# Optimization experiments

Measured on AMD Instinct MI355X. Metric: run time of the kernel, lower is better.

Reference implementation:

```python
import jax, jax.numpy as jnp
import numpy as np

B, C, L = 32, 256, 4096
CM = C // 8  # intermediate channels
EPS = 1e-5


def _conv1x1(v, w, b):
    # v: [B, Cin, L], w: [Cout, Cin], b: [Cout]
    return jnp.einsum('bcl,oc->bol', v, w) + b[None, :, None]


def _bn(v, gamma, beta, mean, var):
    # eval-mode BatchNorm1d over channel dim; v: [B, Ch, L]
    inv = gamma / jnp.sqrt(var + EPS)
    return v * inv[None, :, None] + (beta - mean * inv)[None, :, None]


def setup_inputs() -> dict:
    key = jax.random.key(0)
    ks = jax.random.split(key, 28)
    s = lambda fan: 1.0 / np.sqrt(fan)

    def bn_params(k, ch):
        k1, k2, k3, k4 = jax.random.split(k, 4)
        return (jax.random.normal(k1, (ch,)) * 0.1 + 1.0,   # gamma
                jax.random.normal(k2, (ch,)) * 0.1,          # beta
                jax.random.normal(k3, (ch,)) * 0.1,          # running mean
                jax.random.uniform(k4, (ch,)) + 0.5)         # running var (>0)

    lg1, lbe1, lm1, lv1 = bn_params(ks[2], CM)
    lg2, lbe2, lm2, lv2 = bn_params(ks[5], C)
    gg1, gbe1, gm1, gv1 = bn_params(ks[8], CM)
    gg2, gbe2, gm2, gv2 = bn_params(ks[11], C)

    return dict(
        x=jax.random.normal(ks[0], (B, C, L), dtype=jnp.float32),
        y=jax.random.normal(ks[1], (B, C, L), dtype=jnp.float32),
        lw1=jax.random.uniform(ks[12], (CM, C), minval=-s(C), maxval=s(C)),
        lb1=jax.random.uniform(ks[13], (CM,), minval=-s(C), maxval=s(C)),
        lg1=lg1, lbe1=lbe1, lm1=lm1, lv1=lv1,
        lw2=jax.random.uniform(ks[14], (C, CM), minval=-s(CM), maxval=s(CM)),
        lb2=jax.random.uniform(ks[15], (C,), minval=-s(CM), maxval=s(CM)),
        lg2=lg2, lbe2=lbe2, lm2=lm2, lv2=lv2,
        gw1=jax.random.uniform(ks[16], (CM, C), minval=-s(C), maxval=s(C)),
        gb1=jax.random.uniform(ks[17], (CM,), minval=-s(C), maxval=s(C)),
        gg1=gg1, gbe1=gbe1, gm1=gm1, gv1=gv1,
        gw2=jax.random.uniform(ks[18], (C, CM), minval=-s(CM), maxval=s(CM)),
        gb2=jax.random.uniform(ks[19], (C,), minval=-s(CM), maxval=s(CM)),
        gg2=gg2, gbe2=gbe2, gm2=gm2, gv2=gv2,
    )


def reference(x, y,
              lw1, lb1, lg1, lbe1, lm1, lv1,
              lw2, lb2, lg2, lbe2, lm2, lv2,
              gw1, gb1, gg1, gbe1, gm1, gv1,
              gw2, gb2, gg2, gbe2, gm2, gv2):
    combined = x + y  # [B, C, L]

    # local branch: conv1x1 -> BN -> ReLU -> conv1x1 -> BN
    la = _bn(_conv1x1(combined, lw1, lb1), lg1, lbe1, lm1, lv1)
    la = jax.nn.relu(la)
    la = _bn(_conv1x1(la, lw2, lb2), lg2, lbe2, lm2, lv2)  # [B, C, L]

    # global branch: AdaptiveMaxPool1d(1) -> conv1x1 -> BN -> ReLU -> conv1x1 -> BN
    ga = jnp.max(combined, axis=2, keepdims=True)  # [B, C, 1]
    ga = _bn(_conv1x1(ga, gw1, gb1), gg1, gbe1, gm1, gv1)
    ga = jax.nn.relu(ga)
    ga = _bn(_conv1x1(ga, gw2, gb2), gg2, gbe2, gm2, gv2)  # [B, C, 1]

    att = jax.nn.sigmoid(la + ga)  # broadcast over L
    return 2.0 * x * att + 2.0 * y * (1.0 - att)
```

## Files before the change

### kernel.cpp

```cpp
#include <hip/hip_runtime.h>
#include <hip/hip_bf16.h>


#define NB 32
#define NC 256
#define NM 32
#define NL 4096
#define BNEPS 1e-5f

#define LT1 128
#define KST 128
#define LDW 132
#define LT2 64

typedef unsigned int u32;
typedef unsigned short u16;
typedef __attribute__((ext_vector_type(8))) short bf16x8;
typedef __attribute__((ext_vector_type(4))) float f32x4;

#define OFF_AF1  0
#define OFF_AF2  (OFF_AF1 + 4096)
#define OFF_B1F  (OFF_AF2 + 4096)
#define OFF_B2F  (OFF_B1F + NM)
#define OFF_GW1T (OFF_B2F + NC)
#define OFF_GB1F (OFF_GW1T + NC*NM)
#define OFF_GW2T (OFF_GB1F + NM)
#define OFF_GB2F (OFF_GW2T + NM*NC)
#define OFF_AC   (OFF_GB2F + NC)
#define OFF_GMAX (OFF_AC + NB*NC)
#define OFF_HC   (OFF_GMAX + NB*NC)

__device__ __forceinline__ unsigned f2u_mono(float f) {
    unsigned u = __float_as_uint(f);
    return (u & 0x80000000u) ? ~u : (u | 0x80000000u);
}
__device__ __forceinline__ float u2f_mono(unsigned u) {
    return (u & 0x80000000u) ? __uint_as_float(u & 0x7fffffffu)
                             : __uint_as_float(~u);
}
__device__ __forceinline__ u16 f2bf(float a) {
    return __bfloat16_as_ushort(__float2bfloat16(a));
}
__device__ __forceinline__ float bf2f(u16 a) {
    return __uint_as_float(((u32)a) << 16);
}
__device__ __forceinline__ u32 pack2(float a, float b) {
    return (u32)f2bf(a) | ((u32)f2bf(b) << 16);
}

__global__ __launch_bounds__(256) void k_fold(
    const float* __restrict__ lw1, const float* __restrict__ lb1,
    const float* __restrict__ lg1, const float* __restrict__ lbe1,
    const float* __restrict__ lm1, const float* __restrict__ lv1,
    const float* __restrict__ lw2, const float* __restrict__ lb2,
    const float* __restrict__ lg2, const float* __restrict__ lbe2,
    const float* __restrict__ lm2, const float* __restrict__ lv2,
    const float* __restrict__ gw1, const float* __restrict__ gb1,
    const float* __restrict__ gg1, const float* __restrict__ gbe1,
    const float* __restrict__ gm1, const float* __restrict__ gv1,
    const float* __restrict__ gw2, const float* __restrict__ gb2,
    const float* __restrict__ gg2, const float* __restrict__ gbe2,
    const float* __restrict__ gm2, const float* __restrict__ gv2,
    float* __restrict__ ws) {
    u16* af1   = (u16*)(ws + OFF_AF1);
    u16* af2   = (u16*)(ws + OFF_AF2);
    float* b1f  = ws + OFF_B1F;  float* b2f  = ws + OFF_B2F;
    float* gw1t = ws + OFF_GW1T; float* gb1f = ws + OFF_GB1F;
    float* gw2t = ws + OFF_GW2T; float* gb2f = ws + OFF_GB2F;
    unsigned* gmaxU = (unsigned*)(ws + OFF_GMAX);

    int tid = blockIdx.x * blockDim.x + threadIdx.x;
    int nt  = gridDim.x * blockDim.x;

    for (int i = tid; i < 8192; i += nt) {
        int j = i & 7, lane = (i >> 3) & 63, q = (i >> 9) & 7, mt = i >> 12;
        int m = 16 * mt + (lane & 15);
        int c = 32 * q + 8 * (lane >> 4) + j;
        float inv = lg1[m] * rsqrtf(lv1[m] + BNEPS);
        af1[i] = f2bf(lw1[m * NC + c] * inv);
    }
    for (int i = tid; i < 8192; i += nt) {
        int j = i & 7, lane = (i >> 3) & 63, ct = i >> 9;
        int cout = 16 * ct + (lane & 15);
        int m = 8 * (lane >> 4) + j;
        float inv = lg2[cout] * rsqrtf(lv2[cout] + BNEPS);
        af2[i] = f2bf(lw2[cout * NM + m] * inv);
    }
    for (int i = tid; i < NC * NM; i += nt) {
        int c = i >> 5, m = i & 31;
        float gi1 = gg1[m] * rsqrtf(gv1[m] + BNEPS);
        gw1t[c * NM + m] = gw1[m * NC + c] * gi1;
        float gi2 = gg2[c] * rsqrtf(gv2[c] + BNEPS);
        gw2t[m * NC + c] = gw2[c * NM + m] * gi2;
    }
    for (int i = tid; i < NM; i += nt) {
        float inv = lg1[i] * rsqrtf(lv1[i] + BNEPS);
        b1f[i] = lb1[i] * inv + lbe1[i] - lm1[i] * inv;
        float gi = gg1[i] * rsqrtf(gv1[i] + BNEPS);
        gb1f[i] = gb1[i] * gi + gbe1[i] - gm1[i] * gi;
    }
    for (int i = tid; i < NC; i += nt) {
        float inv = lg2[i] * rsqrtf(lv2[i] + BNEPS);
        b2f[i] = lb2[i] * inv + lbe2[i] - lm2[i] * inv;
        float gi = gg2[i] * rsqrtf(gv2[i] + BNEPS);
        gb2f[i] = gb2[i] * gi + gbe2[i] - gm2[i] * gi;
    }
    for (int i = tid; i < NB * NC; i += nt) gmaxU[i] = 0u;
}

__global__ __launch_bounds__(256, 4) void k_pass1(
    const float4* __restrict__ x4, const float4* __restrict__ y4,
    const u16* __restrict__ af1, const float* __restrict__ b1f,
    unsigned* __restrict__ gmaxU, u16* __restrict__ hc) {
    __shared__ u16 vt[KST * LDW];
    __shared__ float cmax[256];
    int b   = blockIdx.y;
    int l0  = blockIdx.x * LT1;
    int tid = threadIdx.x;
    int w = tid >> 6, lane = tid & 63, g = lane >> 4, li = lane & 15;

    bf16x8 a1[2][8];
#pragma unroll
    for (int mt = 0; mt < 2; ++mt)
#pragma unroll
        for (int q = 0; q < 8; ++q)
            a1[mt][q] = *(const bf16x8*)(af1 + (((mt * 8 + q) * 64) + lane) * 8);

    f32x4 acc[2][2];
#pragma unroll
    for (int mt = 0; mt < 2; ++mt)
#pragma unroll
        for (int t = 0; t < 2; ++t) {
            f32x4 z = {0.f, 0.f, 0.f, 0.f};
            acc[mt][t] = z;
        }

    int hw = tid >> 5;
    int lq = tid & 31;

#pragma unroll
    for (int s = 0; s < 2; ++s) {
#pragma unroll 4
        for (int it = 0; it < 16; ++it) {
            int cc = it * 8 + hw;
            int c  = s * KST + cc;
            size_t ridx = ((size_t)(b * NC + c)) * (NL / 4) + (l0 / 4) + lq;
            float4 xv = x4[ridx];
            float4 yv = y4[ridx];
            float v0 = xv.x + yv.x, v1 = xv.y + yv.y;
            float v2 = xv.z + yv.z, v3 = xv.w + yv.w;
            uint2 wv;
            wv.x = pack2(v0, v1);
            wv.y = pack2(v2, v3);
            *(uint2*)&vt[cc * LDW + 4 * lq] = wv;
        }
        __syncthreads();

#pragma unroll
        for (int qq = 0; qq < 4; ++qq)
#pragma unroll
            for (int t = 0; t < 2; ++t) {
                int lcol = 32 * w + 16 * t + li;
                bf16x8 bf;
#pragma unroll
                for (int j = 0; j < 8; ++j)
                    bf[j] = (short)vt[(32 * qq + 8 * g + j) * LDW + lcol];
                acc[0][t] = __builtin_amdgcn_mfma_f32_16x16x32_bf16(
                    a1[0][s * 4 + qq], bf, acc[0][t], 0, 0, 0);
                acc[1][t] = __builtin_amdgcn_mfma_f32_16x16x32_bf16(
                    a1[1][s * 4 + qq], bf, acc[1][t], 0, 0, 0);
            }

        {
            int cc = tid & 127, half = tid >> 7;
            float mx = -3.402823466e38f;
            int base = cc * LDW + half * 64;
#pragma unroll 8
            for (int l = 0; l < 64; ++l)
                mx = fmaxf(mx, bf2f(vt[base + l]));
            cmax[tid] = mx;
        }
        __syncthreads();
        if (tid < 128)
            atomicMax(&gmaxU[b * NC + s * KST + tid],
                      f2u_mono(fmaxf(cmax[tid], cmax[tid + 128])));
    }

#pragma unroll
    for (int mt = 0; mt < 2; ++mt)
#pragma unroll
        for (int t = 0; t < 2; ++t) {
            int l  = l0 + 32 * w + 16 * t + li;
            int m0 = 16 * mt + 4 * g;
            float h0 = fmaxf(acc[mt][t][0] + b1f[m0 + 0], 0.f);
            float h1 = fmaxf(acc[mt][t][1] + b1f[m0 + 1], 0.f);
            float h2 = fmaxf(acc[mt][t][2] + b1f[m0 + 2], 0.f);
            float h3 = fmaxf(acc[mt][t][3] + b1f[m0 + 3], 0.f);
            uint2 st;
            st.x = pack2(h0, h1);
            st.y = pack2(h2, h3);
            *(uint2*)&hc[((size_t)b * NL + l) * NM + m0] = st;
        }
}

__global__ __launch_bounds__(256) void k_global(
    const float* __restrict__ gw1t, const float* __restrict__ gb1f,
    const float* __restrict__ gw2t, const float* __restrict__ gb2f,
    const float* __restrict__ b2f, const unsigned* __restrict__ gmaxU,
    float* __restrict__ ac) {
    __shared__ float smax[NC];
    __shared__ float g1[NM];
    int b = blockIdx.x;
    int t = threadIdx.x;
    smax[t] = u2f_mono(gmaxU[b * NC + t]);
    __syncthreads();
    if (t < NM) {
        float a = gb1f[t];
        for (int c = 0; c < NC; ++c) a = fmaf(gw1t[c * NM + t], smax[c], a);
        g1[t] = fmaxf(a, 0.f);
    }
    __syncthreads();
    float a = b2f[t] + gb2f[t];
#pragma unroll
    for (int m = 0; m < NM; ++m) a = fmaf(gw2t[m * NC + t], g1[m], a);
    ac[b * NC + t] = a;
}

__global__ __launch_bounds__(256, 4) void k_pass2(
    const float* __restrict__ x, const float* __restrict__ y,
    const u16* __restrict__ af2, const float* __restrict__ ac,
    const u16* __restrict__ hc, float* __restrict__ out) {
    __shared__ float acl[NC];
    int b   = blockIdx.y;
    int l0  = blockIdx.x * LT2;
    int tid = threadIdx.x;
    int w = tid >> 6, lane = tid & 63, g = lane >> 4, li = lane & 15;

    acl[tid] = ac[b * NC + tid];

    bf16x8 a2[4];
#pragma unroll
    for (int ct = 0; ct < 4; ++ct)
        a2[ct] = *(const bf16x8*)(af2 + ((w * 4 + ct) * 64 + lane) * 8);
    __syncthreads();

#pragma unroll 2
    for (int lt = 0; lt < 4; ++lt) {
        int l = l0 + 16 * lt + li;
        bf16x8 bfrag = *(const bf16x8*)(hc + ((size_t)b * NL + l) * NM + 8 * g);
        f32x4 acc[4];
#pragma unroll
        for (int ct = 0; ct < 4; ++ct) {
            f32x4 z = {0.f, 0.f, 0.f, 0.f};
            acc[ct] = __builtin_amdgcn_mfma_f32_16x16x32_bf16(
                a2[ct], bfrag, z, 0, 0, 0);
        }
#pragma unroll
        for (int ct = 0; ct < 4; ++ct)
#pragma unroll
            for (int r = 0; r < 4; ++r) {
                int cout = 64 * w + 16 * ct + 4 * g + r;
                float z = acc[ct][r] + acl[cout];
                float att = 1.f / (1.f + __expf(-z));
                size_t idx = ((size_t)(b * NC + cout)) * NL + l;
                float xv = x[idx];
                float yv = y[idx];
                float tt = yv + att * (xv - yv);
                out[idx] = tt + tt;
            }
    }
}

extern "C" void kernel_launch(void* const* d_in, const int* in_sizes, int n_in,
                              void* d_out, int out_size, void* d_ws,
                              size_t ws_size, hipStream_t stream) {
    (void)in_sizes; (void)n_in; (void)out_size; (void)ws_size;
    const float* x = (const float*)d_in[0];
    const float* y = (const float*)d_in[1];
    float* ws  = (float*)d_ws;
    float* out = (float*)d_out;

    u16* af1   = (u16*)(ws + OFF_AF1);
    u16* af2   = (u16*)(ws + OFF_AF2);
    float* b1f  = ws + OFF_B1F;  float* b2f  = ws + OFF_B2F;
    float* gw1t = ws + OFF_GW1T; float* gb1f = ws + OFF_GB1F;
    float* gw2t = ws + OFF_GW2T; float* gb2f = ws + OFF_GB2F;
    float* ac   = ws + OFF_AC;
    unsigned* gmaxU = (unsigned*)(ws + OFF_GMAX);
    u16* hc = (u16*)(ws + OFF_HC);

    k_fold<<<64, 256, 0, stream>>>(
        (const float*)d_in[2],  (const float*)d_in[3],  (const float*)d_in[4],
        (const float*)d_in[5],  (const float*)d_in[6],  (const float*)d_in[7],
        (const float*)d_in[8],  (const float*)d_in[9],  (const float*)d_in[10],
        (const float*)d_in[11], (const float*)d_in[12], (const float*)d_in[13],
        (const float*)d_in[14], (const float*)d_in[15], (const float*)d_in[16],
        (const float*)d_in[17], (const float*)d_in[18], (const float*)d_in[19],
        (const float*)d_in[20], (const float*)d_in[21], (const float*)d_in[22],
        (const float*)d_in[23], (const float*)d_in[24], (const float*)d_in[25],
        ws);
    k_pass1<<<dim3(NL / LT1, NB), 256, 0, stream>>>(
        (const float4*)x, (const float4*)y, af1, b1f, gmaxU, hc);
    k_global<<<NB, 256, 0, stream>>>(gw1t, gb1f, gw2t, gb2f, b2f, gmaxU, ac);
    k_pass2<<<dim3(NL / LT2, NB), 256, 0, stream>>>(
        x, y, af2, ac, hc, out);
}
```

Measured before the change: 479.2 us.

## Fuse second conv into first pass and stream blend over bf16 pre-activations

The second 1x1 conv now runs inside the first kernel from a shared-memory hidden tile, and the full 256-channel pre-activation is stored as bf16 in channel-major layout. A separate elementwise blend kernel then reads x, y and the pre-activation with vectorized, coalesced float4 loads and applies sigmoid and the mix. The aim is to replace the strided scalar loads of the old second pass with streaming access. In exchange it adds a large intermediate buffer (extra global write and read traffic), and the work is split into batch halves when the workspace is too small.

```diff
diff --git a/kernel.cpp b/kernel.cpp
--- a/kernel.cpp
+++ b/kernel.cpp
@@ -7,11 +7,9 @@
 #define NM 32
 #define NL 4096
 #define BNEPS 1e-5f
-
 #define LT1 128
-#define KST 128
 #define LDW 132
-#define LT2 64
+#define HLW 40
 
 typedef unsigned int u32;
 typedef unsigned short u16;
@@ -28,7 +26,7 @@
 #define OFF_GB2F (OFF_GW2T + NM*NC)
 #define OFF_AC   (OFF_GB2F + NC)
 #define OFF_GMAX (OFF_AC + NB*NC)
-#define OFF_HC   (OFF_GMAX + NB*NC)
+#define OFF_Z    (OFF_GMAX + NB*NC)
 
 __device__ __forceinline__ unsigned f2u_mono(float f) {
     unsigned u = __float_as_uint(f);
@@ -108,56 +106,55 @@
     for (int i = tid; i < NB * NC; i += nt) gmaxU[i] = 0u;
 }
 
-__global__ __launch_bounds__(256, 4) void k_pass1(
+__global__ __launch_bounds__(256, 4) void k_conv(
     const float4* __restrict__ x4, const float4* __restrict__ y4,
-    const u16* __restrict__ af1, const float* __restrict__ b1f,
-    unsigned* __restrict__ gmaxU, u16* __restrict__ hc) {
-    __shared__ u16 vt[KST * LDW];
+    const u16* __restrict__ af1, const u16* __restrict__ af2,
+    const float* __restrict__ b1f, unsigned* __restrict__ gmaxU,
+    u32* __restrict__ z2, int b_off) {
+    __shared__ u16 vt[64 * LDW];
+    __shared__ u16 hl[128 * HLW];
     __shared__ float cmax[256];
-    int b   = blockIdx.y;
-    int l0  = blockIdx.x * LT1;
-    int tid = threadIdx.x;
+    int brel = blockIdx.y;
+    int b    = b_off + brel;
+    int l0   = blockIdx.x * LT1;
+    int tid  = threadIdx.x;
     int w = tid >> 6, lane = tid & 63, g = lane >> 4, li = lane & 15;
-
-    bf16x8 a1[2][8];
+    int hw = tid >> 5, lq = tid & 31;
+
+    f32x4 acc[2][2];
 #pragma unroll
     for (int mt = 0; mt < 2; ++mt)
 #pragma unroll
-        for (int q = 0; q < 8; ++q)
-            a1[mt][q] = *(const bf16x8*)(af1 + (((mt * 8 + q) * 64) + lane) * 8);
-
-    f32x4 acc[2][2];
-#pragma unroll
-    for (int mt = 0; mt < 2; ++mt)
-#pragma unroll
         for (int t = 0; t < 2; ++t) {
-            f32x4 z = {0.f, 0.f, 0.f, 0.f};
-            acc[mt][t] = z;
-        }
-
-    int hw = tid >> 5;
-    int lq = tid & 31;
-
-#pragma unroll
-    for (int s = 0; s < 2; ++s) {
-#pragma unroll 4
-        for (int it = 0; it < 16; ++it) {
+            f32x4 zr = {0.f, 0.f, 0.f, 0.f};
+            acc[mt][t] = zr;
+        }
+
+    for (int s = 0; s < 4; ++s) {
+        bf16x8 a1[2][2];
+#pragma unroll
+        for (int mt = 0; mt < 2; ++mt)
+#pragma unroll
+            for (int qq = 0; qq < 2; ++qq)
+                a1[mt][qq] = *(const bf16x8*)(
+                    af1 + (((mt * 8 + 2 * s + qq) * 64) + lane) * 8);
+
+#pragma unroll
+        for (int it = 0; it < 8; ++it) {
             int cc = it * 8 + hw;
-            int c  = s * KST + cc;
-            size_t ridx = ((size_t)(b * NC + c)) * (NL / 4) + (l0 / 4) + lq;
+            int c  = s * 64 + cc;
+            size_t ridx = ((size_t)(b * NC + c)) * (NL / 4) + (l0 >> 2) + lq;
             float4 xv = x4[ridx];
             float4 yv = y4[ridx];
-            float v0 = xv.x + yv.x, v1 = xv.y + yv.y;
-            float v2 = xv.z + yv.z, v3 = xv.w + yv.w;
             uint2 wv;
-            wv.x = pack2(v0, v1);
-            wv.y = pack2(v2, v3);
+            wv.x = pack2(xv.x + yv.x, xv.y + yv.y);
+            wv.y = pack2(xv.z + yv.z, xv.w + yv.w);
             *(uint2*)&vt[cc * LDW + 4 * lq] = wv;
         }
         __syncthreads();
 
 #pragma unroll
-        for (int qq = 0; qq < 4; ++qq)
+        for (int qq = 0; qq < 2; ++qq)
 #pragma unroll
             for (int t = 0; t < 2; ++t) {
                 int lcol = 32 * w + 16 * t + li;
@@ -166,31 +163,33 @@
                 for (int j = 0; j < 8; ++j)
                     bf[j] = (short)vt[(32 * qq + 8 * g + j) * LDW + lcol];
                 acc[0][t] = __builtin_amdgcn_mfma_f32_16x16x32_bf16(
-                    a1[0][s * 4 + qq], bf, acc[0][t], 0, 0, 0);
+                    a1[0][qq], bf, acc[0][t], 0, 0, 0);
                 acc[1][t] = __builtin_amdgcn_mfma_f32_16x16x32_bf16(
-                    a1[1][s * 4 + qq], bf, acc[1][t], 0, 0, 0);
+                    a1[1][qq], bf, acc[1][t], 0, 0, 0);
             }
 
         {
-            int cc = tid & 127, half = tid >> 7;
+            int cc = tid & 63, q4 = tid >> 6;
+            int base = cc * LDW + 32 * q4;
             float mx = -3.402823466e38f;
-            int base = cc * LDW + half * 64;
 #pragma unroll 8
-            for (int l = 0; l < 64; ++l)
+            for (int l = 0; l < 32; ++l)
                 mx = fmaxf(mx, bf2f(vt[base + l]));
             cmax[tid] = mx;
         }
         __syncthreads();
-        if (tid < 128)
-            atomicMax(&gmaxU[b * NC + s * KST + tid],
-                      f2u_mono(fmaxf(cmax[tid], cmax[tid + 128])));
+        if (tid < 64) {
+            float m0 = fmaxf(fmaxf(cmax[tid], cmax[tid + 64]),
+                             fmaxf(cmax[tid + 128], cmax[tid + 192]));
+            atomicMax(&gmaxU[b * NC + s * 64 + tid], f2u_mono(m0));
+        }
     }
 
 #pragma unroll
     for (int mt = 0; mt < 2; ++mt)
 #pragma unroll
         for (int t = 0; t < 2; ++t) {
-            int l  = l0 + 32 * w + 16 * t + li;
+            int l  = 32 * w + 16 * t + li;
             int m0 = 16 * mt + 4 * g;
             float h0 = fmaxf(acc[mt][t][0] + b1f[m0 + 0], 0.f);
             float h1 = fmaxf(acc[mt][t][1] + b1f[m0 + 1], 0.f);
@@ -199,18 +198,46 @@
             uint2 st;
             st.x = pack2(h0, h1);
             st.y = pack2(h2, h3);
-            *(uint2*)&hc[((size_t)b * NL + l) * NM + m0] = st;
-        }
+            *(uint2*)&hl[l * HLW + m0] = st;
+        }
+    __syncthreads();
+
+    for (int r = 0; r < 4; ++r) {
+#pragma unroll
+        for (int c4 = 0; c4 < 4; ++c4) {
+            int ct = 4 * r + c4;
+            bf16x8 a2 = *(const bf16x8*)(af2 + (ct * 64 + lane) * 8);
+#pragma unroll
+            for (int t = 0; t < 2; ++t) {
+                int l = 32 * w + 16 * t + li;
+                bf16x8 hb = *(const bf16x8*)&hl[l * HLW + 8 * g];
+                f32x4 zz = {0.f, 0.f, 0.f, 0.f};
+                zz = __builtin_amdgcn_mfma_f32_16x16x32_bf16(a2, hb, zz, 0, 0, 0);
+#pragma unroll
+                for (int rr = 0; rr < 4; ++rr)
+                    vt[(16 * c4 + 4 * g + rr) * LDW + l] = f2bf(zz[rr]);
+            }
+        }
+        __syncthreads();
+#pragma unroll
+        for (int i = 0; i < 16; ++i) {
+            int row  = 16 * w + i;
+            int cout = 64 * r + row;
+            u32 v = *(const u32*)&vt[row * LDW + 2 * lane];
+            z2[(((size_t)brel * NC + cout) * NL + l0) / 2 + lane] = v;
+        }
+        __syncthreads();
+    }
 }
 
 __global__ __launch_bounds__(256) void k_global(
     const float* __restrict__ gw1t, const float* __restrict__ gb1f,
     const float* __restrict__ gw2t, const float* __restrict__ gb2f,
     const float* __restrict__ b2f, const unsigned* __restrict__ gmaxU,
-    float* __restrict__ ac) {
+    float* __restrict__ ac, int b_off) {
     __shared__ float smax[NC];
     __shared__ float g1[NM];
-    int b = blockIdx.x;
+    int b = b_off + blockIdx.x;
     int t = threadIdx.x;
     smax[t] = u2f_mono(gmaxU[b * NC + t]);
     __syncthreads();
@@ -226,55 +253,44 @@
     ac[b * NC + t] = a;
 }
 
-__global__ __launch_bounds__(256, 4) void k_pass2(
-    const float* __restrict__ x, const float* __restrict__ y,
-    const u16* __restrict__ af2, const float* __restrict__ ac,
-    const u16* __restrict__ hc, float* __restrict__ out) {
-    __shared__ float acl[NC];
-    int b   = blockIdx.y;
-    int l0  = blockIdx.x * LT2;
-    int tid = threadIdx.x;
-    int w = tid >> 6, lane = tid & 63, g = lane >> 4, li = lane & 15;
-
-    acl[tid] = ac[b * NC + tid];
-
-    bf16x8 a2[4];
-#pragma unroll
-    for (int ct = 0; ct < 4; ++ct)
-        a2[ct] = *(const bf16x8*)(af2 + ((w * 4 + ct) * 64 + lane) * 8);
-    __syncthreads();
-
+__global__ __launch_bounds__(256, 8) void k_blend(
+    const float4* __restrict__ x4, const float4* __restrict__ y4,
+    const uint2* __restrict__ z2, const float* __restrict__ ac,
+    float4* __restrict__ out4, int b_off) {
+    int t0     = blockIdx.x * 256 + threadIdx.x;
+    int stride = gridDim.x * 256;
 #pragma unroll 2
-    for (int lt = 0; lt < 4; ++lt) {
-        int l = l0 + 16 * lt + li;
-        bf16x8 bfrag = *(const bf16x8*)(hc + ((size_t)b * NL + l) * NM + 8 * g);
-        f32x4 acc[4];
-#pragma unroll
-        for (int ct = 0; ct < 4; ++ct) {
-            f32x4 z = {0.f, 0.f, 0.f, 0.f};
-            acc[ct] = __builtin_amdgcn_mfma_f32_16x16x32_bf16(
-                a2[ct], bfrag, z, 0, 0, 0);
-        }
-#pragma unroll
-        for (int ct = 0; ct < 4; ++ct)
-#pragma unroll
-            for (int r = 0; r < 4; ++r) {
-                int cout = 64 * w + 16 * ct + 4 * g + r;
-                float z = acc[ct][r] + acl[cout];
-                float att = 1.f / (1.f + __expf(-z));
-                size_t idx = ((size_t)(b * NC + cout)) * NL + l;
-                float xv = x[idx];
-                float yv = y[idx];
-                float tt = yv + att * (xv - yv);
-                out[idx] = tt + tt;
-            }
+    for (int it = 0; it < 16; ++it) {
+        int f = t0 + it * stride;
+        int brel = f >> 18;
+        int c    = (f >> 10) & (NC - 1);
+        size_t fg = ((size_t)b_off << 18) + f;
+        float4 xv = x4[fg];
+        float4 yv = y4[fg];
+        uint2  zv = z2[f];
+        float a = ac[(b_off + brel) * NC + c];
+        float z0 = bf2f((u16)(zv.x & 0xffffu)) + a;
+        float z1 = bf2f((u16)(zv.x >> 16)) + a;
+        float z2v = bf2f((u16)(zv.y & 0xffffu)) + a;
+        float z3 = bf2f((u16)(zv.y >> 16)) + a;
+        float a0 = 1.f / (1.f + __expf(-z0));
+        float a1 = 1.f / (1.f + __expf(-z1));
+        float a2 = 1.f / (1.f + __expf(-z2v));
+        float a3 = 1.f / (1.f + __expf(-z3));
+        float4 o;
+        float t;
+        t = yv.x + a0 * (xv.x - yv.x); o.x = t + t;
+        t = yv.y + a1 * (xv.y - yv.y); o.y = t + t;
+        t = yv.z + a2 * (xv.z - yv.z); o.z = t + t;
+        t = yv.w + a3 * (xv.w - yv.w); o.w = t + t;
+        out4[fg] = o;
     }
 }
 
 extern "C" void kernel_launch(void* const* d_in, const int* in_sizes, int n_in,
                               void* d_out, int out_size, void* d_ws,
                               size_t ws_size, hipStream_t stream) {
-    (void)in_sizes; (void)n_in; (void)out_size; (void)ws_size;
+    (void)in_sizes; (void)n_in; (void)out_size;
     const float* x = (const float*)d_in[0];
     const float* y = (const float*)d_in[1];
     float* ws  = (float*)d_ws;
@@ -287,7 +303,7 @@
     float* gw2t = ws + OFF_GW2T; float* gb2f = ws + OFF_GB2F;
     float* ac   = ws + OFF_AC;
     unsigned* gmaxU = (unsigned*)(ws + OFF_GMAX);
-    u16* hc = (u16*)(ws + OFF_HC);
+    u32* z2 = (u32*)(ws + OFF_Z);
 
     k_fold<<<64, 256, 0, stream>>>(
         (const float*)d_in[2],  (const float*)d_in[3],  (const float*)d_in[4],
@@ -299,9 +315,17 @@
         (const float*)d_in[20], (const float*)d_in[21], (const float*)d_in[22],
         (const float*)d_in[23], (const float*)d_in[24], (const float*)d_in[25],
         ws);
-    k_pass1<<<dim3(NL / LT1, NB), 256, 0, stream>>>(
-        (const float4*)x, (const float4*)y, af1, b1f, gmaxU, hc);
-    k_global<<<NB, 256, 0, stream>>>(gw1t, gb1f, gw2t, gb2f, b2f, gmaxU, ac);
-    k_pass2<<<dim3(NL / LT2, NB), 256, 0, stream>>>(
-        x, y, af2, ac, hc, out);
-}
+
+    size_t need_full = ((size_t)OFF_Z + (size_t)NB * NC * NL / 2) * 4;
+    int nbh = (ws_size >= need_full) ? NB : (NB / 2);
+
+    for (int b0 = 0; b0 < NB; b0 += nbh) {
+        k_conv<<<dim3(NL / LT1, nbh), 256, 0, stream>>>(
+            (const float4*)x, (const float4*)y, af1, af2, b1f, gmaxU, z2, b0);
+        k_global<<<nbh, 256, 0, stream>>>(
+            gw1t, gb1f, gw2t, gb2f, b2f, gmaxU, ac, b0);
+        k_blend<<<nbh * 64, 256, 0, stream>>>(
+            (const float4*)x, (const float4*)y, (const uint2*)z2, ac,
+            (float4*)out, b0);
+    }
+}
```

After: 448.2 us. -6.5%, faster.
